# Optimization experiments

Hardware: AMD Instinct MI355X
Metric: run time of the kernel (lower is better)

## Reference

```python
import jax, jax.numpy as jnp
import numpy as np

B_, L_, D_, H_ = 2, 1024, 1024, 16


def _matrixR(L, d_model):
    # Transformer-XL sinusoid table, reversed along the position axis (reverse=True)
    inv_freq = 1.0 / (10000.0 ** (np.arange(0, d_model, 2, dtype=np.float32) / d_model))
    sinus = np.arange(L, dtype=np.float32)[:, None] * inv_freq[None, :]
    mat = np.zeros((L, d_model), dtype=np.float32)
    mat[:, 0::2] = np.sin(sinus)
    mat[:, 1::2] = np.cos(sinus)
    return jnp.asarray(mat[::-1].copy())


def _shift_b(x):
    # x: (b, h, L, L) -> TXL relative shift + lower-triangular mask
    b, h, L, _ = x.shape
    pad = jnp.concatenate([jnp.zeros((b, h, L, 1), x.dtype), x], axis=-1)  # (b,h,L,L+1)
    shifted = pad.reshape(b, h, L + 1, L)[:, :, 1:, :]                      # (b,h,L,L)
    return jnp.tril(shifted)


def setup_inputs() -> dict:
    key = jax.random.key(0)
    ks = jax.random.split(key, 8)
    s = 1.0 / np.sqrt(D_)
    return {
        "E": jax.random.normal(ks[0], (B_, L_, D_), dtype=jnp.float32),
        "Ev": jax.random.normal(ks[1], (B_, L_, D_), dtype=jnp.float32),
        "R": _matrixR(L_, D_),
        "Wq": jax.random.normal(ks[2], (D_, D_), dtype=jnp.float32) * s,
        "Wke": jax.random.normal(ks[3], (D_, D_), dtype=jnp.float32) * s,
        "Wkr": jax.random.normal(ks[4], (D_, D_), dtype=jnp.float32) * s,
        "Wv": jax.random.normal(ks[5], (D_, D_), dtype=jnp.float32) * s,
        "cb": jnp.ones((D_,), dtype=jnp.float32),
        "pb": jnp.ones((D_,), dtype=jnp.float32),
        "Wo_w": jax.random.normal(ks[6], (D_, D_), dtype=jnp.float32) * s,
        "Wo_b": jnp.zeros((D_,), dtype=jnp.float32),
        "ln_g": jnp.ones((D_,), dtype=jnp.float32),
        "ln_b": jnp.zeros((D_,), dtype=jnp.float32),
    }


def reference(E, Ev, R, Wq, Wke, Wkr, Wv, cb, pb, Wo_w, Wo_b, ln_g, ln_b):
    b, L, d = E.shape
    h = H_
    dh = d // h
    # projections -> (b, h, L, dh)
    q = (E @ Wq).reshape(b, L, h, dh).transpose(0, 2, 1, 3)
    k = (Ev @ Wke).reshape(b, L, h, dh).transpose(0, 2, 1, 3)
    v = (Ev @ Wv).reshape(b, L, h, dh).transpose(0, 2, 1, 3)
    # relative-position keys (batch independent): (h, L, dh)
    Q = (R @ Wkr).reshape(L, h, dh).transpose(1, 0, 2)
    # (a) content-content
    A_a = jnp.einsum('bhid,bhjd->bhij', q, k)
    # (b) content-position, with shift trick
    A_b = _shift_b(jnp.einsum('bhid,hjd->bhij', q, Q))
    # (c) global content bias (same for every query row)
    A_c = jnp.einsum('hd,bhjd->bhj', cb.reshape(h, dh), k)[:, :, None, :]  # (b,h,1,L)
    # (d) global position bias (batch independent), shifted
    d_row = jnp.einsum('hd,hjd->hj', pb.reshape(h, dh), Q)                 # (h,L)
    A_d = _shift_b(jnp.broadcast_to(d_row[None, :, None, :], (1, h, L, L)))
    A = A_a + A_b + A_c + A_d
    p = jax.nn.softmax(A, axis=-1)
    Oh = jnp.einsum('bhij,bhjd->bhid', p, v)
    O = Oh.transpose(0, 2, 1, 3).reshape(b, L, d)
    # residual + output proj (dropout is identity in eval) + LayerNorm
    res = Ev + (O @ Wo_w + Wo_b)
    mu = jnp.mean(res, axis=-1, keepdims=True)
    var = jnp.mean((res - mu) ** 2, axis=-1, keepdims=True)
    return (res - mu) * jax.lax.rsqrt(var + 1e-5) * ln_g + ln_b
```

## Files before the change

kernel.cpp:

```cpp
#include <hip/hip_runtime.h>
#include <hip/hip_bf16.h>
#include <math.h>

#define B_ 2
#define L_ 1024
#define D_ 1024
#define H_ 16

typedef short short8 __attribute__((ext_vector_type(8)));
typedef short short4v __attribute__((ext_vector_type(4)));
typedef float f32x4  __attribute__((ext_vector_type(4)));

__device__ __forceinline__ short f2bf(float f) {
  unsigned u = __float_as_uint(f);
  u += 0x7fff + ((u >> 16) & 1);
  return (short)(u >> 16);
}
__device__ __forceinline__ float bf2f(short s) {
  return __uint_as_float(((unsigned)(unsigned short)s) << 16);
}
__device__ __forceinline__ int swz(int row, int slot) {
  return row * 64 + (((slot ^ row) & 7) << 3);
}
__device__ __forceinline__ int pkey(int row) {
  return (row & 7) ^ ((row & 8) >> 2);
}
__device__ __forceinline__ void glds16(const void* g, void* l) {
  __builtin_amdgcn_global_load_lds((const __attribute__((address_space(1))) void*)g,
                                   (__attribute__((address_space(3))) void*)l, 16, 0, 0);
}

__global__ __launch_bounds__(256) void prep(
    const float* __restrict__ E, const float* __restrict__ Ev,
    const float* __restrict__ R,
    const float* __restrict__ W0, const float* __restrict__ W1,
    const float* __restrict__ W2, const float* __restrict__ W3,
    const float* __restrict__ W4,
    short* __restrict__ act, short* __restrict__ Wt) {
  __shared__ short t[64][65];
  const int tid = threadIdx.x;
  int bid = blockIdx.x;
  if (bid < 2560) {
    size_t i8 = ((size_t)bid * 256 + tid) * 8;
    const float* src; size_t off;
    if (i8 < 2097152)      { src = E;  off = i8; }
    else if (i8 < 4194304) { src = Ev; off = i8 - 2097152; }
    else                   { src = R;  off = i8 - 4194304; }
    float4 a = *(const float4*)&src[off];
    float4 b = *(const float4*)&src[off + 4];
    short8 v;
    v[0] = f2bf(a.x); v[1] = f2bf(a.y); v[2] = f2bf(a.z); v[3] = f2bf(a.w);
    v[4] = f2bf(b.x); v[5] = f2bf(b.y); v[6] = f2bf(b.z); v[7] = f2bf(b.w);
    *(short8*)&act[i8] = v;
    return;
  }
  bid -= 2560;
  const int z = bid >> 8, rem = bid & 255;
  const int by = rem >> 4, bx = rem & 15;
  const float* W = (z == 0) ? W0 : (z == 1) ? W1 : (z == 2) ? W2 : (z == 3) ? W3 : W4;
  short* Wtz = Wt + (size_t)z * D_ * D_;
  const int r0 = by * 64, c0 = bx * 64;
  #pragma unroll
  for (int i = 0; i < 4; ++i) {
    int idx = tid + i * 256;
    int r = idx >> 4, c4 = (idx & 15) * 4;
    float4 v = *(const float4*)&W[(size_t)(r0 + r) * D_ + c0 + c4];
    t[c4 + 0][r] = f2bf(v.x); t[c4 + 1][r] = f2bf(v.y);
    t[c4 + 2][r] = f2bf(v.z); t[c4 + 3][r] = f2bf(v.w);
  }
  __syncthreads();
  #pragma unroll
  for (int i = 0; i < 2; ++i) {
    int idx = tid + i * 256;
    int rr = idx >> 3, cc = (idx & 7) * 8;
    short8 o;
    #pragma unroll
    for (int e = 0; e < 8; ++e) o[e] = t[rr][cc + e];
    *(short8*)&Wtz[(size_t)(c0 + rr) * D_ + r0 + cc] = o;
  }
}

template<int NF, int OUT>
__device__ __forceinline__ void mm_db(const short* __restrict__ A,
                                      const short* __restrict__ Bt,
                                      void* __restrict__ Cp,
                                      int bx, int by) {
  __shared__ short As0[4096], As1[4096];
  __shared__ short Bs0[NF * 2048], Bs1[NF * 2048];
  const int tid = threadIdx.x;
  const int l = tid & 63, w = tid >> 6;
  const int row0 = by * 64, col0 = bx * (NF * 32);
  const int wm = (w >> 1) * 32, wn = (w & 1) * (NF * 16);
  const int lr = l >> 3;
  const int lc = ((l & 7) ^ lr) * 8;
  const f32x4 fz = {0.f, 0.f, 0.f, 0.f};

  f32x4 acc[2][NF];
  #pragma unroll
  for (int i = 0; i < 2; ++i)
    #pragma unroll
    for (int j = 0; j < NF; ++j) acc[i][j] = fz;

  auto STAGE = [&](short* AsD, short* BsD, int k0) {
    #pragma unroll
    for (int c = 0; c < 2; ++c) {
      int ch = w * 2 + c;
      glds16(&A[(size_t)(row0 + ch * 8 + lr) * 1024 + k0 + lc], &AsD[ch * 512]);
    }
    #pragma unroll
    for (int c = 0; c < NF; ++c) {
      int ch = w * NF + c;
      glds16(&Bt[(size_t)(col0 + ch * 8 + lr) * 1024 + k0 + lc], &BsD[ch * 512]);
    }
  };
  auto COMP = [&](const short* AsS, const short* BsS) {
    #pragma unroll
    for (int kf = 0; kf < 2; ++kf) {
      const int slot = kf * 4 + (l >> 4);
      short8 a[2], bfr[NF];
      #pragma unroll
      for (int mf = 0; mf < 2; ++mf)
        a[mf] = *(const short8*)&AsS[swz(wm + mf * 16 + (l & 15), slot)];
      #pragma unroll
      for (int nf = 0; nf < NF; ++nf)
        bfr[nf] = *(const short8*)&BsS[swz(wn + nf * 16 + (l & 15), slot)];
      #pragma unroll
      for (int mf = 0; mf < 2; ++mf)
        #pragma unroll
        for (int nf = 0; nf < NF; ++nf)
          acc[mf][nf] = __builtin_amdgcn_mfma_f32_16x16x32_bf16(a[mf], bfr[nf], acc[mf][nf], 0, 0, 0);
    }
  };

  STAGE(As0, Bs0, 0);
  __syncthreads();
  for (int t = 0; t < 16; t += 2) {
    if (t + 1 < 16) STAGE(As1, Bs1, (t + 1) * 64);
    COMP(As0, Bs0);
    __syncthreads();
    if (t + 2 < 16) STAGE(As0, Bs0, (t + 2) * 64);
    COMP(As1, Bs1);
    __syncthreads();
  }

  #pragma unroll
  for (int mf = 0; mf < 2; ++mf)
    #pragma unroll
    for (int nf = 0; nf < NF; ++nf) {
      if (OUT == 2) {
        int tok = row0 + wm + mf * 16 + (l >> 4) * 4;
        int col = col0 + wn + nf * 16 + (l & 15);
        int bb = tok >> 10, j = tok & 1023;
        int h = col >> 6, d = col & 63;
        short4v o;
        #pragma unroll
        for (int r = 0; r < 4; ++r) o[r] = f2bf(acc[mf][nf][r]);
        *(short4v*)&((short*)Cp)[((size_t)((bb * H_ + h) * 64 + d)) * 1024 + j] = o;
      } else {
        #pragma unroll
        for (int r = 0; r < 4; ++r) {
          int row = row0 + wm + mf * 16 + (l >> 4) * 4 + r;
          int col = col0 + wn + nf * 16 + (l & 15);
          if (OUT == 1) ((float*)Cp)[(size_t)row * 1024 + col] = acc[mf][nf][r];
          else          ((short*)Cp)[(size_t)row * 1024 + col] = f2bf(acc[mf][nf][r]);
        }
      }
    }
}

__global__ __launch_bounds__(256) void proj_g(
    const short* __restrict__ Eb, const short* __restrict__ Evb,
    const short* __restrict__ Rb, const short* __restrict__ Wt,
    short* __restrict__ qb, short* __restrict__ kb,
    short* __restrict__ vt, short* __restrict__ Qpb) {
  const int z = blockIdx.z;
  const size_t MM = (size_t)D_ * D_;
  const short* A; const short* Bt; short* C; int M;
  if (z == 0)      { A = Eb;  Bt = Wt;          C = qb;  M = B_ * L_; }
  else if (z == 1) { A = Evb; Bt = Wt + MM;     C = kb;  M = B_ * L_; }
  else if (z == 2) { A = Evb; Bt = Wt + 3 * MM; C = vt;  M = B_ * L_; }
  else             { A = Rb;  Bt = Wt + 2 * MM; C = Qpb; M = L_;      }
  if ((int)blockIdx.y * 64 >= M) return;
  if (z == 2) mm_db<4, 2>(A, Bt, C, blockIdx.x, blockIdx.y);
  else        mm_db<4, 0>(A, Bt, C, blockIdx.x, blockIdx.y);
}

__global__ __launch_bounds__(256) void out_g(
    const short* __restrict__ Ob, const short* __restrict__ Wot,
    float* __restrict__ proj) {
  mm_db<2, 1>(Ob, Wot, proj, blockIdx.x, blockIdx.y);
}

__global__ __launch_bounds__(256, 3) void attn_s(
    const short* __restrict__ qb, const short* __restrict__ kb,
    const short* __restrict__ vt, const short* __restrict__ Qpb,
    const float* __restrict__ cb, const float* __restrict__ pb,
    short* __restrict__ Ob) {
  __shared__ short k_s0[4096], k_s1[4096];
  __shared__ short vt_s0[4096], vt_s1[4096];
  __shared__ short pbs[4 * 1312];

  const int tid = threadIdx.x;
  const int l = tid & 63, w = tid >> 6;
  const int hl = blockIdx.x & 31;
  const int it = blockIdx.x >> 5;
  const int b = hl >> 4, hh = hl & 15;
  const int i0 = it * 64;
  const int i0w = i0 + w * 16;
  const f32x4 fz = {0.f, 0.f, 0.f, 0.f};

  const int lr = l >> 3;
  const int lc = ((l & 7) ^ lr) * 8;

  short8 aqc[2], aqp[2];
  {
    const size_t qoff = (size_t)(b * L_ + i0w + (l & 15)) * D_ + hh * 64 + (l >> 4) * 8;
    #pragma unroll
    for (int kf = 0; kf < 2; ++kf) {
      short8 qv = *(const short8*)&qb[qoff + kf * 32];
      const float* cbp = &cb[hh * 64 + kf * 32 + (l >> 4) * 8];
      const float* pbp = &pb[hh * 64 + kf * 32 + (l >> 4) * 8];
      #pragma unroll
      for (int e = 0; e < 8; ++e) {
        float q = bf2f(qv[e]);
        aqc[kf][e] = f2bf(q + cbp[e]);
        aqp[kf][e] = f2bf(q + pbp[e]);
      }
    }
  }

  const short* kbase  = &kb[(size_t)(b * L_) * D_ + hh * 64];
  const short* vtbase = &vt[(size_t)((b * H_ + hh) * 64) * 1024];
  const short* wbase  = &Qpb[hh * 64 + (l >> 4) * 8];

  auto STAGE = [&](short* kD, short* vD, int jt) {
    const int j0 = jt * 64;
    #pragma unroll
    for (int c = 0; c < 2; ++c) {
      int ch = w * 2 + c;
      glds16(&kbase[(size_t)(j0 + ch * 8 + lr) * D_ + lc], &kD[ch * 512]);
      glds16(&vtbase[(size_t)(ch * 8 + lr) * 1024 + j0 + lc], &vD[ch * 512]);
    }
  };

  short8 bw[2][5];
  auto LW = [&](int jt) {
    const int mb = L_ - 16 - (i0w - jt * 64);
    #pragma unroll
    for (int kf = 0; kf < 2; ++kf)
      #pragma unroll
      for (int u = 0; u < 5; ++u) {
        int m = mb + u * 16 + (l & 15);
        m = (m < L_) ? m : (L_ - 1);
        bw[kf][u] = *(const short8*)&wbase[(size_t)m * D_ + kf * 32];
      }
  };

  STAGE(k_s0, vt_s0, 0);
  LW(0);
  __syncthreads();

  float mrow[4], lrow[4];
  f32x4 oacc[4];
  #pragma unroll
  for (int r = 0; r < 4; ++r) { mrow[r] = -3.0e38f; lrow[r] = 0.f; }
  #pragma unroll
  for (int nf = 0; nf < 4; ++nf) oacc[nf] = fz;

  const int pbb = w * 1312;

  for (int jt = 0; jt < 16; ++jt) {
    const int dth = i0w - jt * 64;
    const bool pos = (dth >= -15);
    const short* kS  = (jt & 1) ? k_s1 : k_s0;
    const short* vS  = (jt & 1) ? vt_s1 : vt_s0;
    short* kD = (jt & 1) ? k_s0 : k_s1;
    short* vD = (jt & 1) ? vt_s0 : vt_s1;

    if (jt < 15) STAGE(kD, vD, jt + 1);

    f32x4 sac[4];
    #pragma unroll
    for (int nf = 0; nf < 4; ++nf) sac[nf] = fz;
    __builtin_amdgcn_s_setprio(1);
    #pragma unroll
    for (int kf = 0; kf < 2; ++kf) {
      const int slot = kf * 4 + (l >> 4);
      #pragma unroll
      for (int nf = 0; nf < 4; ++nf) {
        short8 bk = *(const short8*)&kS[swz(nf * 16 + (l & 15), slot)];
        sac[nf] = __builtin_amdgcn_mfma_f32_16x16x32_bf16(aqc[kf], bk, sac[nf], 0, 0, 0);
      }
    }
    __builtin_amdgcn_s_setprio(0);

    if (pos) {
      f32x4 pacc[5];
      #pragma unroll
      for (int u = 0; u < 5; ++u) pacc[u] = fz;
      __builtin_amdgcn_s_setprio(1);
      #pragma unroll
      for (int kf = 0; kf < 2; ++kf)
        #pragma unroll
        for (int u = 0; u < 5; ++u)
          pacc[u] = __builtin_amdgcn_mfma_f32_16x16x32_bf16(aqp[kf], bw[kf][u], pacc[u], 0, 0, 0);
      __builtin_amdgcn_s_setprio(0);
      #pragma unroll
      for (int u = 0; u < 5; ++u)
        #pragma unroll
        for (int r = 0; r < 4; ++r) {
          int row = (l >> 4) * 4 + r;
          pbs[pbb + row * 82 + u * 16 + (l & 15)] = f2bf(pacc[u][r]);
        }
    }

    if (jt < 15 && dth - 64 >= -15) LW(jt + 1);

    if (pos) {
      #pragma unroll
      for (int nf = 0; nf < 4; ++nf)
        #pragma unroll
        for (int r = 0; r < 4; ++r) {
          int ris = (l >> 4) * 4 + r;
          int rj = nf * 16 + (l & 15);
          if (rj <= ris + dth)
            sac[nf][r] += bf2f(pbs[pbb + ris * 82 + (15 - ris + rj)]);
        }
    }

    #pragma unroll
    for (int r = 0; r < 4; ++r) {
      float mx = fmaxf(fmaxf(sac[0][r], sac[1][r]), fmaxf(sac[2][r], sac[3][r]));
      #pragma unroll
      for (int off = 1; off < 16; off <<= 1)
        mx = fmaxf(mx, __shfl_xor(mx, off, 64));
      float mn = fmaxf(mrow[r], mx);
      float sc = __expf(mrow[r] - mn);
      mrow[r] = mn;
      float ls = 0.f;
      #pragma unroll
      for (int nf = 0; nf < 4; ++nf) {
        float p = __expf(sac[nf][r] - mn);
        sac[nf][r] = p;
        ls += p;
      }
      #pragma unroll
      for (int off = 1; off < 16; off <<= 1)
        ls += __shfl_xor(ls, off, 64);
      lrow[r] = lrow[r] * sc + ls;
      #pragma unroll
      for (int nf = 0; nf < 4; ++nf) oacc[nf][r] *= sc;
    }

    #pragma unroll
    for (int nf = 0; nf < 4; ++nf)
      #pragma unroll
      for (int r = 0; r < 4; ++r) {
        int row = (l >> 4) * 4 + r;
        int col = nf * 16 + (l & 15);
        pbs[pbb + row * 64 + (((col >> 3) ^ pkey(row)) << 3) + (col & 7)] = f2bf(sac[nf][r]);
      }

    __builtin_amdgcn_s_setprio(1);
    #pragma unroll
    for (int kf = 0; kf < 2; ++kf) {
      int prow = l & 15;
      short8 ap = *(const short8*)&pbs[pbb + prow * 64 + (((kf * 4 + (l >> 4)) ^ pkey(prow)) << 3)];
      #pragma unroll
      for (int nf = 0; nf < 4; ++nf) {
        short8 bv = *(const short8*)&vS[swz(nf * 16 + (l & 15), kf * 4 + (l >> 4))];
        oacc[nf] = __builtin_amdgcn_mfma_f32_16x16x32_bf16(ap, bv, oacc[nf], 0, 0, 0);
      }
    }
    __builtin_amdgcn_s_setprio(0);

    __syncthreads();
  }

  #pragma unroll
  for (int r = 0; r < 4; ++r) {
    float inv = 1.f / lrow[r];
    #pragma unroll
    for (int nf = 0; nf < 4; ++nf) {
      int row = i0w + (l >> 4) * 4 + r;
      int col = hh * 64 + nf * 16 + (l & 15);
      Ob[(size_t)(b * L_ + row) * D_ + col] = f2bf(oacc[nf][r] * inv);
    }
  }
}

__global__ __launch_bounds__(256) void ln_kernel(
    const float* __restrict__ Ev, const float* __restrict__ proj,
    const float* __restrict__ Wo_b, const float* __restrict__ g,
    const float* __restrict__ beta, float* __restrict__ out) {
  const int row = blockIdx.x;
  __shared__ float red[8];
  const int tid = threadIdx.x;
  const int d = tid * 4;

  float4 e  = *(const float4*)&Ev[(size_t)row * D_ + d];
  float4 p  = *(const float4*)&proj[(size_t)row * D_ + d];
  float4 wb = *(const float4*)&Wo_b[d];
  float4 rr = { e.x + p.x + wb.x, e.y + p.y + wb.y,
                e.z + p.z + wb.z, e.w + p.w + wb.w };
  float sum = rr.x + rr.y + rr.z + rr.w;
  float sq  = rr.x * rr.x + rr.y * rr.y + rr.z * rr.z + rr.w * rr.w;

  #pragma unroll
  for (int off = 1; off < 64; off <<= 1) {
    sum += __shfl_xor(sum, off, 64);
    sq  += __shfl_xor(sq,  off, 64);
  }
  const int wid = tid >> 6;
  if ((tid & 63) == 0) { red[wid * 2] = sum; red[wid * 2 + 1] = sq; }
  __syncthreads();
  sum = red[0] + red[2] + red[4] + red[6];
  sq  = red[1] + red[3] + red[5] + red[7];

  const float mu   = sum * (1.f / (float)D_);
  const float var  = sq * (1.f / (float)D_) - mu * mu;
  const float rstd = rsqrtf(var + 1e-5f);

  float4 gg = *(const float4*)&g[d];
  float4 bb = *(const float4*)&beta[d];
  float4 o = { (rr.x - mu) * rstd * gg.x + bb.x,
               (rr.y - mu) * rstd * gg.y + bb.y,
               (rr.z - mu) * rstd * gg.z + bb.z,
               (rr.w - mu) * rstd * gg.w + bb.w };
  *(float4*)&out[(size_t)row * D_ + d] = o;
}

extern "C" void kernel_launch(void* const* d_in, const int* in_sizes, int n_in,
                              void* d_out, int out_size, void* d_ws, size_t ws_size,
                              hipStream_t stream) {
  const float* E    = (const float*)d_in[0];
  const float* Ev   = (const float*)d_in[1];
  const float* R    = (const float*)d_in[2];
  const float* Wq   = (const float*)d_in[3];
  const float* Wke  = (const float*)d_in[4];
  const float* Wkr  = (const float*)d_in[5];
  const float* Wv   = (const float*)d_in[6];
  const float* cb   = (const float*)d_in[7];
  const float* pb   = (const float*)d_in[8];
  const float* Wo_w = (const float*)d_in[9];
  const float* Wo_b = (const float*)d_in[10];
  const float* ln_g = (const float*)d_in[11];
  const float* ln_b = (const float*)d_in[12];
  float* out = (float*)d_out;

  short* ws   = (short*)d_ws;
  short* Eb   = ws;
  short* Evb  = ws + 2097152;
  short* Rb   = ws + 4194304;
  short* qb   = ws + 5242880;
  short* kb   = ws + 7340032;
  short* vt   = ws + 9437184;
  short* Qpb  = ws + 11534336;
  short* Wt   = ws + 12582912;
  short* Ob   = ws + 17825792;
  float* proj = (float*)Eb;

  prep<<<3840, 256, 0, stream>>>(E, Ev, R, Wq, Wke, Wkr, Wv, Wo_w, Eb, Wt);

  proj_g<<<dim3(8, 32, 4), 256, 0, stream>>>(Eb, Evb, Rb, Wt, qb, kb, vt, Qpb);

  attn_s<<<512, 256, 0, stream>>>(qb, kb, vt, Qpb, cb, pb, Ob);

  out_g<<<dim3(16, 32), 256, 0, stream>>>(Ob, Wt + 4 * (size_t)D_ * D_, proj);

  ln_kernel<<<B_ * L_, 256, 0, stream>>>(Ev, proj, Wo_b, ln_g, ln_b, out);
}
```

Baseline: 224.0 us.

## Split attention key range across two wave groups and merge partial softmax

The attention kernel now runs 512 threads per block: two groups of four waves each process alternating 64-key tiles and stage two tiles per round, then merge their partial softmax states through shared memory at the end. The relative-position shift is now done with cross-lane shuffles instead of a round trip through shared memory. The projection GEMM switches to a smaller tile template with twice as many blocks in x. The aim is more parallel waves per block and less LDS traffic, at the cost of an extra merge step and higher shared-memory use per block.

```diff
diff --git a/kernel.cpp b/kernel.cpp
--- a/kernel.cpp
+++ b/kernel.cpp
@@ -181,8 +181,8 @@
   else if (z == 2) { A = Evb; Bt = Wt + 3 * MM; C = vt;  M = B_ * L_; }
   else             { A = Rb;  Bt = Wt + 2 * MM; C = Qpb; M = L_;      }
   if ((int)blockIdx.y * 64 >= M) return;
-  if (z == 2) mm_db<4, 2>(A, Bt, C, blockIdx.x, blockIdx.y);
-  else        mm_db<4, 0>(A, Bt, C, blockIdx.x, blockIdx.y);
+  if (z == 2) mm_db<2, 2>(A, Bt, C, blockIdx.x, blockIdx.y);
+  else        mm_db<2, 0>(A, Bt, C, blockIdx.x, blockIdx.y);
 }
 
 __global__ __launch_bounds__(256) void out_g(
@@ -191,22 +191,23 @@
   mm_db<2, 1>(Ob, Wot, proj, blockIdx.x, blockIdx.y);
 }
 
-__global__ __launch_bounds__(256, 3) void attn_s(
+__global__ __launch_bounds__(512, 4) void attn_s(
     const short* __restrict__ qb, const short* __restrict__ kb,
     const short* __restrict__ vt, const short* __restrict__ Qpb,
     const float* __restrict__ cb, const float* __restrict__ pb,
     short* __restrict__ Ob) {
-  __shared__ short k_s0[4096], k_s1[4096];
-  __shared__ short vt_s0[4096], vt_s1[4096];
-  __shared__ short pbs[4 * 1312];
+  __shared__ short k_s[2][2][4096];
+  __shared__ short v_s[2][2][4096];
+  __shared__ short p_s[8][1024];
 
   const int tid = threadIdx.x;
   const int l = tid & 63, w = tid >> 6;
+  const int grp = w >> 2, wl = w & 3;
   const int hl = blockIdx.x & 31;
   const int it = blockIdx.x >> 5;
   const int b = hl >> 4, hh = hl & 15;
   const int i0 = it * 64;
-  const int i0w = i0 + w * 16;
+  const int i0w = i0 + wl * 16;
   const f32x4 fz = {0.f, 0.f, 0.f, 0.f};
 
   const int lr = l >> 3;
@@ -233,13 +234,12 @@
   const short* vtbase = &vt[(size_t)((b * H_ + hh) * 64) * 1024];
   const short* wbase  = &Qpb[hh * 64 + (l >> 4) * 8];
 
-  auto STAGE = [&](short* kD, short* vD, int jt) {
-    const int j0 = jt * 64;
-    #pragma unroll
-    for (int c = 0; c < 2; ++c) {
-      int ch = w * 2 + c;
-      glds16(&kbase[(size_t)(j0 + ch * 8 + lr) * D_ + lc], &kD[ch * 512]);
-      glds16(&vtbase[(size_t)(ch * 8 + lr) * 1024 + j0 + lc], &vD[ch * 512]);
+  auto STAGE = [&](int buf, int rnd) {
+    #pragma unroll
+    for (int tp = 0; tp < 2; ++tp) {
+      const int j0 = (2 * rnd + tp) * 64;
+      glds16(&kbase[(size_t)(j0 + w * 8 + lr) * D_ + lc], &k_s[buf][tp][w * 512]);
+      glds16(&vtbase[(size_t)(w * 8 + lr) * 1024 + j0 + lc], &v_s[buf][tp][w * 512]);
     }
   };
 
@@ -256,8 +256,8 @@
       }
   };
 
-  STAGE(k_s0, vt_s0, 0);
-  LW(0);
+  STAGE(0, 0);
+  if (i0w - grp * 64 >= -15) LW(grp);
   __syncthreads();
 
   float mrow[4], lrow[4];
@@ -267,17 +267,14 @@
   #pragma unroll
   for (int nf = 0; nf < 4; ++nf) oacc[nf] = fz;
 
-  const int pbb = w * 1312;
-
-  for (int jt = 0; jt < 16; ++jt) {
+  for (int rnd = 0; rnd < 8; ++rnd) {
+    const int jt = 2 * rnd + grp;
     const int dth = i0w - jt * 64;
     const bool pos = (dth >= -15);
-    const short* kS  = (jt & 1) ? k_s1 : k_s0;
-    const short* vS  = (jt & 1) ? vt_s1 : vt_s0;
-    short* kD = (jt & 1) ? k_s0 : k_s1;
-    short* vD = (jt & 1) ? vt_s0 : vt_s1;
-
-    if (jt < 15) STAGE(kD, vD, jt + 1);
+    const short* kS = k_s[rnd & 1][grp];
+    const short* vS = v_s[rnd & 1][grp];
+
+    if (rnd < 7) STAGE((rnd + 1) & 1, rnd + 1);
 
     f32x4 sac[4];
     #pragma unroll
@@ -294,8 +291,8 @@
     }
     __builtin_amdgcn_s_setprio(0);
 
+    f32x4 pacc[5];
     if (pos) {
-      f32x4 pacc[5];
       #pragma unroll
       for (int u = 0; u < 5; ++u) pacc[u] = fz;
       __builtin_amdgcn_s_setprio(1);
@@ -305,27 +302,27 @@
         for (int u = 0; u < 5; ++u)
           pacc[u] = __builtin_amdgcn_mfma_f32_16x16x32_bf16(aqp[kf], bw[kf][u], pacc[u], 0, 0, 0);
       __builtin_amdgcn_s_setprio(0);
-      #pragma unroll
-      for (int u = 0; u < 5; ++u)
-        #pragma unroll
-        for (int r = 0; r < 4; ++r) {
-          int row = (l >> 4) * 4 + r;
-          pbs[pbb + row * 82 + u * 16 + (l & 15)] = f2bf(pacc[u][r]);
+    }
+
+    if (rnd < 7 && dth - 128 >= -15) LW(jt + 2);
+
+    if (pos) {
+      const int c = l & 15;
+      #pragma unroll
+      for (int r = 0; r < 4; ++r) {
+        const int ris = (l >> 4) * 4 + r;
+        const int t = (15 - ris) + c;
+        const int sl = (l & 48) | (t & 15);
+        const bool hi = t >= 16;
+        float shf[5];
+        #pragma unroll
+        for (int u = 0; u < 5; ++u) shf[u] = __shfl(pacc[u][r], sl, 64);
+        #pragma unroll
+        for (int nf = 0; nf < 4; ++nf) {
+          int rj = nf * 16 + c;
+          if (rj <= ris + dth) sac[nf][r] += hi ? shf[nf + 1] : shf[nf];
         }
-    }
-
-    if (jt < 15 && dth - 64 >= -15) LW(jt + 1);
-
-    if (pos) {
-      #pragma unroll
-      for (int nf = 0; nf < 4; ++nf)
-        #pragma unroll
-        for (int r = 0; r < 4; ++r) {
-          int ris = (l >> 4) * 4 + r;
-          int rj = nf * 16 + (l & 15);
-          if (rj <= ris + dth)
-            sac[nf][r] += bf2f(pbs[pbb + ris * 82 + (15 - ris + rj)]);
-        }
+      }
     }
 
     #pragma unroll
@@ -358,14 +355,14 @@
       for (int r = 0; r < 4; ++r) {
         int row = (l >> 4) * 4 + r;
         int col = nf * 16 + (l & 15);
-        pbs[pbb + row * 64 + (((col >> 3) ^ pkey(row)) << 3) + (col & 7)] = f2bf(sac[nf][r]);
+        p_s[w][row * 64 + (((col >> 3) ^ pkey(row)) << 3) + (col & 7)] = f2bf(sac[nf][r]);
       }
 
     __builtin_amdgcn_s_setprio(1);
     #pragma unroll
     for (int kf = 0; kf < 2; ++kf) {
       int prow = l & 15;
-      short8 ap = *(const short8*)&pbs[pbb + prow * 64 + (((kf * 4 + (l >> 4)) ^ pkey(prow)) << 3)];
+      short8 ap = *(const short8*)&p_s[w][prow * 64 + (((kf * 4 + (l >> 4)) ^ pkey(prow)) << 3)];
       #pragma unroll
       for (int nf = 0; nf < 4; ++nf) {
         short8 bv = *(const short8*)&vS[swz(nf * 16 + (l & 15), kf * 4 + (l >> 4))];
@@ -377,14 +374,35 @@
     __syncthreads();
   }
 
-  #pragma unroll
-  for (int r = 0; r < 4; ++r) {
-    float inv = 1.f / lrow[r];
-    #pragma unroll
-    for (int nf = 0; nf < 4; ++nf) {
-      int row = i0w + (l >> 4) * 4 + r;
-      int col = hh * 64 + nf * 16 + (l & 15);
-      Ob[(size_t)(b * L_ + row) * D_ + col] = f2bf(oacc[nf][r] * inv);
+  float* mO = (float*)&k_s[0][0][0];
+  float* mM = (float*)&v_s[0][0][0];
+  float* mL = mM + 64;
+  if (grp == 1) {
+    #pragma unroll
+    for (int r = 0; r < 4; ++r) {
+      int ris = (l >> 4) * 4 + r;
+      #pragma unroll
+      for (int nf = 0; nf < 4; ++nf)
+        mO[(wl * 16 + ris) * 64 + nf * 16 + (l & 15)] = oacc[nf][r];
+      if ((l & 15) == 0) { mM[wl * 16 + ris] = mrow[r]; mL[wl * 16 + ris] = lrow[r]; }
+    }
+  }
+  __syncthreads();
+  if (grp == 0) {
+    #pragma unroll
+    for (int r = 0; r < 4; ++r) {
+      int ris = (l >> 4) * 4 + r;
+      float mB = mM[wl * 16 + ris], lB = mL[wl * 16 + ris];
+      float m = fmaxf(mrow[r], mB);
+      float eA = __expf(mrow[r] - m), eB = __expf(mB - m);
+      float inv = 1.f / (lrow[r] * eA + lB * eB);
+      int row = i0w + ris;
+      #pragma unroll
+      for (int nf = 0; nf < 4; ++nf) {
+        float vB = mO[(wl * 16 + ris) * 64 + nf * 16 + (l & 15)];
+        int col = hh * 64 + nf * 16 + (l & 15);
+        Ob[(size_t)(b * L_ + row) * D_ + col] = f2bf((oacc[nf][r] * eA + vB * eB) * inv);
+      }
     }
   }
 }
@@ -462,9 +480,9 @@
 
   prep<<<3840, 256, 0, stream>>>(E, Ev, R, Wq, Wke, Wkr, Wv, Wo_w, Eb, Wt);
 
-  proj_g<<<dim3(8, 32, 4), 256, 0, stream>>>(Eb, Evb, Rb, Wt, qb, kb, vt, Qpb);
-
-  attn_s<<<512, 256, 0, stream>>>(qb, kb, vt, Qpb, cb, pb, Ob);
+  proj_g<<<dim3(16, 32, 4), 256, 0, stream>>>(Eb, Evb, Rb, Wt, qb, kb, vt, Qpb);
+
+  attn_s<<<512, 512, 0, stream>>>(qb, kb, vt, Qpb, cb, pb, Ob);
 
   out_g<<<dim3(16, 32), 256, 0, stream>>>(Ob, Wt + 4 * (size_t)D_ * D_, proj);
 
```

After: 270.7 us. +20.8%, slower.
